# Performance work log

Measured on AMD Instinct MI355X. Metric: run time of the kernel, lower is better.

The kernel has to match this reference:

```python
import jax, jax.numpy as jnp
import numpy as np

DIM = 2048
HEADS = 16
HD = DIM // HEADS
B = 1
S = 2560
L_CAP = 256
NAG_SCALE = 5.0
NAG_ALPHA = 0.25
NAG_TAU = 2.5
EPS_RMS = 1e-5


def setup_inputs() -> dict:
    key = jax.random.key(0)
    ks = jax.random.split(key, 6)
    h = jax.random.normal(ks[0], (B, S, DIM), dtype=jnp.float32)
    wq = jax.random.normal(ks[1], (DIM, DIM), dtype=jnp.float32) * 0.02
    wk = jax.random.normal(ks[2], (DIM, DIM), dtype=jnp.float32) * 0.02
    wv = jax.random.normal(ks[3], (DIM, DIM), dtype=jnp.float32) * 0.02
    wo = jax.random.normal(ks[4], (DIM, DIM), dtype=jnp.float32) * 0.02
    norm_q_w = jnp.ones((HD,), dtype=jnp.float32)
    norm_k_w = jnp.ones((HD,), dtype=jnp.float32)
    # real rotary angles: freqs_cis[b, s, d, 0]=cos, [...,1]=sin
    pos = jnp.arange(S, dtype=jnp.float32)[:, None]          # [S,1]
    inv_freq = 1.0 / (10000.0 ** (jnp.arange(HD // 2, dtype=jnp.float32) / (HD // 2)))
    ang = pos * inv_freq                                      # [S, HD/2]
    freqs_cis = jnp.stack([jnp.cos(ang), jnp.sin(ang)], axis=-1)[None]  # [1,S,HD/2,2]
    return {"h": h, "wq": wq, "wk": wk, "wv": wv, "wo": wo,
            "norm_q_w": norm_q_w, "norm_k_w": norm_k_w,
            "freqs_cis": freqs_cis, "cap_embed_len": L_CAP}


def _rmsnorm(x, w):
    # over last (head) dim
    return x * jax.lax.rsqrt(jnp.mean(x * x, axis=-1, keepdims=True) + EPS_RMS) * w


def _rope(x, freqs_cis):
    # x: [B,S,H,D]; freqs_cis: [1,S,D/2,2]
    xr = x.reshape(*x.shape[:-1], -1, 2)      # [B,S,H,D/2,2]
    cos = freqs_cis[..., 0][:, :, None, :]    # [1,S,1,D/2]
    sin = freqs_cis[..., 1][:, :, None, :]
    x0, x1 = xr[..., 0], xr[..., 1]
    o0 = x0 * cos - x1 * sin
    o1 = x1 * cos + x0 * sin
    return jnp.stack([o0, o1], axis=-1).reshape(x.shape)


def _sdpa(q, k, v):
    # q,k,v: [B,N,H,D] -> [B,N,H*D]
    scale = 1.0 / jnp.sqrt(jnp.asarray(q.shape[-1], q.dtype))
    s = jnp.einsum('bnhd,bmhd->bhnm', q, k) * scale
    a = jax.nn.softmax(s, axis=-1)
    o = jnp.einsum('bhnm,bmhd->bnhd', a, v)
    return o.reshape(o.shape[0], o.shape[1], -1)


def reference(h, wq, wk, wv, wo, norm_q_w, norm_k_w, freqs_cis, cap_embed_len):
    b, s, dim = h.shape
    q = (h @ wq.T).reshape(b, s, HEADS, HD)
    k = (h @ wk.T).reshape(b, s, HEADS, HD)
    v = (h @ wv.T).reshape(b, s, HEADS, HD)
    q = _rmsnorm(q, norm_q_w)
    k = _rmsnorm(k, norm_k_w)
    q = _rope(q, freqs_cis)
    k = _rope(k, freqs_cis)

    L = cap_embed_len
    # positive pass: drop trailing negative-caption tokens
    x_pos = _sdpa(q[:, :-L], k[:, :-L], v[:, :-L])            # [B,S-L,DIM]
    # swap positive caption slot for the negative caption
    q2 = q.at[:, -2 * L:-L].set(q[:, -L:])
    k2 = k.at[:, -2 * L:-L].set(k[:, -L:])
    v2 = v.at[:, -2 * L:-L].set(v[:, -L:])
    x_neg = _sdpa(q2[:, :-L], k2[:, :-L], v2[:, :-L])         # [B,S-L,DIM]
    x_neg_tail = x_neg[:, -L:]

    x_g = x_neg * (1.0 - NAG_SCALE) + x_pos * NAG_SCALE
    norm_pos = jnp.sum(jnp.abs(x_pos), axis=-1, keepdims=True)
    norm_g = jnp.sum(jnp.abs(x_g), axis=-1, keepdims=True)
    ratio = jnp.nan_to_num(norm_g / norm_pos, nan=10.0)
    factor = (1.0 / (norm_g + 1e-7)) * norm_pos * NAG_TAU
    x_g = jnp.where(ratio > NAG_TAU, x_g * factor, x_g)
    x_g = x_g * NAG_ALPHA + x_pos * (1.0 - NAG_ALPHA)

    out = jnp.concatenate([x_g, x_neg_tail], axis=1)          # [B,S,DIM]
    return out @ wo.T
```

## Files before the change

kernel.cpp:

```cpp
#include <hip/hip_runtime.h>
#include <stdint.h>


typedef short s8x __attribute__((ext_vector_type(8)));
typedef float f4x __attribute__((ext_vector_type(4)));
typedef unsigned short u16;

#define NDIM   2048
#define NHEAD  16
#define NHD    128
#define NSEQ   2560
#define NSDPA  2304

__device__ __forceinline__ u16 f2bf(float f) {
  union { float f; unsigned u; } v; v.f = f;
  unsigned r = v.u + 0x7FFFu + ((v.u >> 16) & 1u);
  return (u16)(r >> 16);
}

__device__ __forceinline__ float bf2f(unsigned hi16_in_place) {
  union { unsigned u; float f; } v; v.u = hi16_in_place;
  return v.f;
}

__device__ __forceinline__ void gload16(const void* g, void* l) {
  __builtin_amdgcn_global_load_lds(
      (const __attribute__((address_space(1))) unsigned*)g,
      (__attribute__((address_space(3))) unsigned*)l, 16, 0, 0);
}

__global__ void k_cast(const float* __restrict__ h, const float* __restrict__ w0,
                       const float* __restrict__ w1, const float* __restrict__ w2,
                       const float* __restrict__ w3, u16* __restrict__ hB,
                       u16* __restrict__ wB) {
  int bid = blockIdx.x;
  const float* src; u16* dst; int i;
  if (bid < 2560) {
    src = h; dst = hB; i = bid * 256 + threadIdx.x;
  } else {
    int b = bid - 2560;
    int m = b >> 11;
    i = (b & 2047) * 256 + threadIdx.x;
    src = (m == 0) ? w0 : (m == 1) ? w1 : (m == 2) ? w2 : w3;
    dst = wB + (size_t)m * 4194304;
  }
  const float4* s4 = (const float4*)src + (size_t)i * 2;
  float4 a = s4[0], b4 = s4[1];
  uint4 p;
  p.x = (unsigned)f2bf(a.x) | ((unsigned)f2bf(a.y) << 16);
  p.y = (unsigned)f2bf(a.z) | ((unsigned)f2bf(a.w) << 16);
  p.z = (unsigned)f2bf(b4.x) | ((unsigned)f2bf(b4.y) << 16);
  p.w = (unsigned)f2bf(b4.z) | ((unsigned)f2bf(b4.w) << 16);
  *(uint4*)(dst + (size_t)i * 8) = p;
}

__global__ __launch_bounds__(256, 2)
void k_gemm_bt(const u16* __restrict__ A, const u16* __restrict__ B,
               float* __restrict__ C, int K, int ldc, int nbn) {
  __shared__ __align__(16) unsigned char sm[16384];
  const int cpx = gridDim.x >> 3;
  const int f = blockIdx.x;
  const int swz = (f & 7) * cpx + (f >> 3);
  const int bm = (swz / nbn) * 128, bn = (swz % nbn) * 128;
  const int lane = threadIdx.x & 63, wl = threadIdx.x >> 6;
  const int wm = wl >> 1, wn = wl & 1;
  const int g = lane >> 4, li = lane & 15;
  f4x acc[4][4] = {};
  const int nk = K >> 5;
  for (int kk = 0; kk < nk; ++kk) {
#pragma unroll
    for (int c = 0; c < 2; ++c) {
      int base = (wl * 2 + c) * 1024;
      int row = (base >> 6) + (lane >> 2);
      int colb = (lane & 3) * 16;
      gload16((const char*)A + ((size_t)(bm + row) * K + kk * 32) * 2 + colb, sm + base);
      gload16((const char*)B + ((size_t)(bn + row) * K + kk * 32) * 2 + colb, sm + 8192 + base);
    }
    __syncthreads();
    s8x a[4];
#pragma unroll
    for (int mt = 0; mt < 4; ++mt)
      a[mt] = *(const s8x*)(sm + (wm * 64 + mt * 16 + li) * 64 + g * 16);
#pragma unroll
    for (int nt = 0; nt < 4; ++nt) {
      s8x b = *(const s8x*)(sm + 8192 + (wn * 64 + nt * 16 + li) * 64 + g * 16);
#pragma unroll
      for (int mt = 0; mt < 4; ++mt)
        acc[mt][nt] = __builtin_amdgcn_mfma_f32_16x16x32_bf16(a[mt], b, acc[mt][nt], 0, 0, 0);
    }
    __syncthreads();
  }
#pragma unroll
  for (int mt = 0; mt < 4; ++mt)
#pragma unroll
    for (int nt = 0; nt < 4; ++nt)
#pragma unroll
      for (int r = 0; r < 4; ++r) {
        int row = bm + wm * 64 + mt * 16 + g * 4 + r;
        int col = bn + wn * 64 + nt * 16 + li;
        C[(size_t)row * ldc + col] = acc[mt][nt][r];
      }
}

__device__ __forceinline__ void stageAB256(const u16* __restrict__ M, int K,
                                           int row0, int kk, unsigned char* dst,
                                           int tid) {
#pragma unroll
  for (int c = 0; c < 4; ++c) {
    int idx = c * 512 + tid;
    int r = idx >> 3, cc = idx & 7;
    gload16(M + (size_t)(row0 + r) * K + kk + ((cc ^ (r & 7)) * 8), dst + idx * 16);
  }
}

#define G256_SYNC() do { __builtin_amdgcn_s_barrier();                        \
    asm volatile("s_waitcnt lgkmcnt(0)" ::: "memory");                        \
    __builtin_amdgcn_sched_barrier(0); } while (0)

__global__ __launch_bounds__(512, 2)
void k_gemm256(const u16* __restrict__ A, const u16* __restrict__ B,
               u16* __restrict__ C, u16* __restrict__ vT,
               int K, int ldc, int nbn) {
  extern __shared__ __align__(16) unsigned char sm[];
  const int tid = threadIdx.x;
  const int lane = tid & 63, wid = tid >> 6;
  const int g = lane >> 4, li = lane & 15;
  const int wr = wid >> 2, wc = wid & 3;

  const int cpx = gridDim.x >> 3;
  const int f = blockIdx.x;
  const int swz = (f & 7) * cpx + (f >> 3);
  const int bm = (swz / nbn) * 256, bn = (swz % nbn) * 256;

  f4x acc[8][4] = {};
  const int nk = K >> 6;

  stageAB256(A, K, bm, 0, sm, tid);
  stageAB256(B, K, bn, 0, sm + 32768, tid);
  stageAB256(A, K, bm, 64, sm + 65536, tid);
  stageAB256(B, K, bn, 64, sm + 98304, tid);
  asm volatile("s_waitcnt vmcnt(8)" ::: "memory");
  __builtin_amdgcn_s_barrier();

  for (int t = 0; t < nk; ++t) {
    unsigned char* sA = sm + (t & 1) * 65536;
    unsigned char* sB = sA + 32768;
    s8x a[8][2], b[4][2];

#pragma unroll
    for (int mt = 0; mt < 4; ++mt) {
      int r = wr * 128 + mt * 16 + li;
#pragma unroll
      for (int ks = 0; ks < 2; ++ks)
        a[mt][ks] = *(const s8x*)(sA + r * 128 + (((ks * 4 + g) ^ (r & 7)) * 16));
    }
#pragma unroll
    for (int nt = 0; nt < 4; ++nt) {
      int r = wc * 64 + nt * 16 + li;
      b[nt][0] = *(const s8x*)(sB + r * 128 + ((g ^ (r & 7)) * 16));
    }
    G256_SYNC();
    __builtin_amdgcn_s_setprio(1);
#pragma unroll
    for (int nt = 0; nt < 4; ++nt)
#pragma unroll
      for (int mt = 0; mt < 4; ++mt)
        acc[mt][nt] = __builtin_amdgcn_mfma_f32_16x16x32_bf16(a[mt][0], b[nt][0], acc[mt][nt], 0, 0, 0);
    __builtin_amdgcn_s_setprio(0);
    __builtin_amdgcn_s_barrier();

#pragma unroll
    for (int mt = 4; mt < 8; ++mt) {
      int r = wr * 128 + mt * 16 + li;
#pragma unroll
      for (int ks = 0; ks < 2; ++ks)
        a[mt][ks] = *(const s8x*)(sA + r * 128 + (((ks * 4 + g) ^ (r & 7)) * 16));
    }
#pragma unroll
    for (int nt = 0; nt < 4; ++nt) {
      int r = wc * 64 + nt * 16 + li;
      b[nt][1] = *(const s8x*)(sB + r * 128 + (((4 + g) ^ (r & 7)) * 16));
    }
    G256_SYNC();
    __builtin_amdgcn_s_setprio(1);
#pragma unroll
    for (int nt = 0; nt < 4; ++nt)
#pragma unroll
      for (int mt = 4; mt < 8; ++mt)
        acc[mt][nt] = __builtin_amdgcn_mfma_f32_16x16x32_bf16(a[mt][0], b[nt][0], acc[mt][nt], 0, 0, 0);
    __builtin_amdgcn_s_setprio(0);
    __builtin_amdgcn_s_barrier();

    if (t + 2 < nk) stageAB256(A, K, bm, (t + 2) * 64, sA, tid);
    G256_SYNC();
    __builtin_amdgcn_s_setprio(1);
#pragma unroll
    for (int nt = 0; nt < 4; ++nt)
#pragma unroll
      for (int mt = 0; mt < 4; ++mt)
        acc[mt][nt] = __builtin_amdgcn_mfma_f32_16x16x32_bf16(a[mt][1], b[nt][1], acc[mt][nt], 0, 0, 0);
    __builtin_amdgcn_s_setprio(0);
    __builtin_amdgcn_s_barrier();

    if (t + 2 < nk) stageAB256(B, K, bn, (t + 2) * 64, sB, tid);
    G256_SYNC();
    __builtin_amdgcn_s_setprio(1);
#pragma unroll
    for (int nt = 0; nt < 4; ++nt)
#pragma unroll
      for (int mt = 4; mt < 8; ++mt)
        acc[mt][nt] = __builtin_amdgcn_mfma_f32_16x16x32_bf16(a[mt][1], b[nt][1], acc[mt][nt], 0, 0, 0);
    __builtin_amdgcn_s_setprio(0);
    if (t + 1 < nk) {
      if (t + 2 < nk) asm volatile("s_waitcnt vmcnt(8)" ::: "memory");
      else            asm volatile("s_waitcnt vmcnt(0)" ::: "memory");
      __builtin_amdgcn_s_barrier();
    }
  }

  if (bn < 4096) {
#pragma unroll
    for (int mt = 0; mt < 8; ++mt)
#pragma unroll
      for (int nt = 0; nt < 4; ++nt)
#pragma unroll
        for (int rr = 0; rr < 4; ++rr) {
          int row = bm + wr * 128 + mt * 16 + g * 4 + rr;
          int col = bn + wc * 64 + nt * 16 + li;
          C[(size_t)row * ldc + col] = f2bf(acc[mt][nt][rr]);
        }
  } else {
    __syncthreads();
#pragma unroll
    for (int mt = 0; mt < 8; ++mt)
#pragma unroll
      for (int nt = 0; nt < 4; ++nt) {
        int col = wc * 64 + nt * 16 + li;
        int rowb = (wr * 128 + mt * 16 + g * 4) * 2;
        u16 pk[4];
#pragma unroll
        for (int rr = 0; rr < 4; ++rr) pk[rr] = f2bf(acc[mt][nt][rr]);
        uint2 w;
        w.x = (unsigned)pk[0] | ((unsigned)pk[1] << 16);
        w.y = (unsigned)pk[2] | ((unsigned)pk[3] << 16);
        *(uint2*)(sm + col * 512 + (rowb ^ ((col & 7) << 4))) = w;
      }
    __syncthreads();
    const int hbase = (bn - 4096) >> 7;
#pragma unroll
    for (int c = 0; c < 16; ++c) {
      int idx = c * 512 + tid;
      int col = idx >> 5, ch = idx & 31;
      uint4 v = *(const uint4*)(sm + col * 512 + ((ch * 16) ^ ((col & 7) << 4)));
      int hh = hbase + (col >> 7);
      int d = col & 127;
      *(uint4*)(vT + ((size_t)hh * 128 + d) * NSEQ + bm + ch * 8) = v;
    }
  }
}

__global__ void k_prep(const u16* __restrict__ qkv, const float* __restrict__ nqw,
                       const float* __restrict__ nkw, const float* __restrict__ fc,
                       u16* __restrict__ qh, u16* __restrict__ kh) {
  int wid = threadIdx.x >> 6, lane = threadIdx.x & 63;
  int pair = blockIdx.x * 4 + wid;
  int s = pair >> 4, hh = pair & 15;
  const u16* qrow = qkv + (size_t)s * 6144 + hh * 128;
  unsigned uq = *(const unsigned*)(qrow + lane * 2);
  unsigned uk = *(const unsigned*)(qrow + 2048 + lane * 2);
  float qx = bf2f(uq << 16), qy = bf2f(uq & 0xFFFF0000u);
  float kx = bf2f(uk << 16), ky = bf2f(uk & 0xFFFF0000u);
  float sq = qx * qx + qy * qy;
  float sk = kx * kx + ky * ky;
#pragma unroll
  for (int m = 32; m >= 1; m >>= 1) { sq += __shfl_xor(sq, m); sk += __shfl_xor(sk, m); }
  float rq = rsqrtf(sq * (1.f / 128.f) + 1e-5f);
  float rk = rsqrtf(sk * (1.f / 128.f) + 1e-5f);
  float2 wq2 = *(const float2*)(nqw + lane * 2);
  float2 wk2 = *(const float2*)(nkw + lane * 2);
  float2 cs = *(const float2*)(fc + (size_t)s * 128 + lane * 2);
  float q0 = qx * rq * wq2.x, q1 = qy * rq * wq2.y;
  float k0 = kx * rk * wk2.x, k1 = ky * rk * wk2.y;
  unsigned qo = (unsigned)f2bf(q0 * cs.x - q1 * cs.y) | ((unsigned)f2bf(q1 * cs.x + q0 * cs.y) << 16);
  unsigned ko = (unsigned)f2bf(k0 * cs.x - k1 * cs.y) | ((unsigned)f2bf(k1 * cs.x + k0 * cs.y) << 16);
  *(unsigned*)(qh + ((size_t)hh * NSEQ + s) * 128 + lane * 2) = qo;
  *(unsigned*)(kh + ((size_t)hh * NSEQ + s) * 128 + lane * 2) = ko;
}

__device__ __forceinline__ void stage_kv(const u16* __restrict__ khh,
                                         const u16* __restrict__ vTh,
                                         int kphys, unsigned char* sm,
                                         int lane, int wl) {
#pragma unroll
  for (int c = 0; c < 4; ++c) {
    int base = (wl * 4 + c) * 1024;
    { int row = (base >> 8) + (lane >> 4);
      int src = ((lane & 15) * 16) ^ ((row & 7) << 4);
      gload16((const char*)(khh + (size_t)(kphys + row) * 128) + src, sm + base); }
    { int row = (base >> 7) + (lane >> 3);
      int src = ((lane & 7) * 16) ^ ((row & 7) << 4);
      gload16((const char*)(vTh + (size_t)row * NSEQ + kphys) + src, sm + 16384 + base); }
  }
}

__device__ __forceinline__ void tile_compute(unsigned char* sm, unsigned char* pb,
                                             const s8x (&aq)[4], int g, int li,
                                             f4x (&o)[9], float& mold) {
  const float S2 = 0.08838834764831845f * 1.4426950408889634f;
  const float THR_RAW = 90.0f;
  const s8x PONE = {16256, 16256, 16256, 16256, 16256, 16256, 16256, 16256};
  const f4x zf = {0.f, 0.f, 0.f, 0.f};
  f4x sc[4];
#pragma unroll
  for (int nt = 0; nt < 4; ++nt) sc[nt] = zf;
  __builtin_amdgcn_s_setprio(1);
#pragma unroll
  for (int nt = 0; nt < 4; ++nt) {
    int row = nt * 16 + li;
    int rx = (row & 7) << 4;
#pragma unroll
    for (int ds = 0; ds < 4; ++ds) {
      s8x bk = *(const s8x*)(sm + row * 256 + ((ds * 64 + g * 16) ^ rx));
      sc[nt] = __builtin_amdgcn_mfma_f32_16x16x32_bf16(bk, aq[ds], sc[nt], 0, 0, 0);
    }
  }
  __builtin_amdgcn_s_setprio(0);

  float tl = fmaxf(fmaxf(fmaxf(sc[0][0], sc[0][1]), fmaxf(sc[0][2], sc[0][3])),
                   fmaxf(fmaxf(sc[1][0], sc[1][1]), fmaxf(sc[1][2], sc[1][3])));
  tl = fmaxf(tl, fmaxf(fmaxf(fmaxf(sc[2][0], sc[2][1]), fmaxf(sc[2][2], sc[2][3])),
                       fmaxf(fmaxf(sc[3][0], sc[3][1]), fmaxf(sc[3][2], sc[3][3]))));
  tl = fmaxf(tl, __shfl_xor(tl, 16));
  tl = fmaxf(tl, __shfl_xor(tl, 32));
  if (__any((int)(tl > mold + THR_RAW))) {
    float mn = fmaxf(mold, tl);
    float corr = exp2f((mold - mn) * S2);
    mold = mn;
    float cf[4];
#pragma unroll
    for (int r = 0; r < 4; ++r)
      cf[r] = __shfl(corr, (g << 4) | (g * 4 + r));
#pragma unroll
    for (int dt = 0; dt < 9; ++dt)
#pragma unroll
      for (int r = 0; r < 4; ++r) o[dt][r] *= cf[r];
  }
  float nb = -mold * S2;
#pragma unroll
  for (int nt = 0; nt < 4; ++nt) {
    u16 pp[4];
#pragma unroll
    for (int r = 0; r < 4; ++r) {
      float p = exp2f(fmaf(sc[nt][r], S2, nb));
      union { float f; unsigned u; } pv_; pv_.f = p;
      pp[r] = (u16)(pv_.u >> 16);
    }
    uint2 w;
    w.x = (unsigned)pp[0] | ((unsigned)pp[1] << 16);
    w.y = (unsigned)pp[2] | ((unsigned)pp[3] << 16);
    *(uint2*)(pb + li * 128 + ((nt * 32 + g * 8) ^ ((li & 7) << 4))) = w;
  }
  __builtin_amdgcn_s_setprio(1);
#pragma unroll
  for (int ks = 0; ks < 2; ++ks) {
    s8x pa = *(const s8x*)(pb + li * 128 + ((ks * 64 + g * 16) ^ ((li & 7) << 4)));
#pragma unroll
    for (int dt = 0; dt < 8; ++dt) {
      int row = dt * 16 + li;
      s8x bv = *(const s8x*)(sm + 16384 + row * 128 + ((ks * 64 + g * 16) ^ ((row & 7) << 4)));
      o[dt] = __builtin_amdgcn_mfma_f32_16x16x32_bf16(pa, bv, o[dt], 0, 0, 0);
    }
    o[8] = __builtin_amdgcn_mfma_f32_16x16x32_bf16(pa, PONE, o[8], 0, 0, 0);
  }
  __builtin_amdgcn_s_setprio(0);
}

__device__ __forceinline__ void epilogue(u16* __restrict__ out, int q0, int hh,
                                         int g, int li, const f4x (&o)[9]) {
  float inv[4];
#pragma unroll
  for (int r = 0; r < 4; ++r) inv[r] = 1.f / o[8][r];
#pragma unroll
  for (int dt = 0; dt < 8; ++dt)
#pragma unroll
    for (int r = 0; r < 4; ++r) {
      int n = q0 + g * 4 + r;
      int col = hh * 128 + dt * 16 + li;
      out[(size_t)n * NDIM + col] = f2bf(o[dt][r] * inv[r]);
    }
}

__global__ __launch_bounds__(256, 3)
void k_attn(const u16* __restrict__ qh, const u16* __restrict__ kh,
            const u16* __restrict__ vT, u16* __restrict__ xpos,
            u16* __restrict__ xneg) {
  __shared__ __align__(16) unsigned char sm[40960];
  const int lane = threadIdx.x & 63, wl = threadIdx.x >> 6;
  const int g = lane >> 4, li = lane & 15;

  const int s = blockIdx.x;
  const int xcd = s & 7, j = s >> 3;
  const int hh = 2 * xcd + (j & 1);
  const int u = j >> 1;
  const bool shared_blk = (u < 32);
  const int qb = shared_blk ? u : (32 + ((u - 32) >> 1));
  const int mode = shared_blk ? 0 : ((u - 32) & 1);
  const int q0 = qb * 64 + wl * 16;

  const u16* khh = kh + (size_t)hh * NSEQ * 128;
  const u16* vTh = vT + (size_t)hh * 128 * NSEQ;
  unsigned char* pb = sm + 32768 + wl * 2048;

  s8x aq[4];
  {
    int ql = q0 + li;
    int qp = (mode && ql >= 2048) ? ql + 256 : ql;
    const u16* base = qh + ((size_t)hh * NSEQ + qp) * 128 + g * 8;
#pragma unroll
    for (int ds = 0; ds < 4; ++ds) aq[ds] = *(const s8x*)(base + ds * 32);
  }

  const f4x zf = {0.f, 0.f, 0.f, 0.f};
  f4x o1[9];
  float m1 = -1e30f;
#pragma unroll
  for (int dt = 0; dt < 9; ++dt) o1[dt] = zf;

  const int n1 = shared_blk ? 32 : 36;
  for (int t = 0; t < n1; ++t) {
    int kphys = (mode && t >= 32) ? 2304 + (t - 32) * 64 : t * 64;
    stage_kv(khh, vTh, kphys, sm, lane, wl);
    __syncthreads();
    tile_compute(sm, pb, aq, g, li, o1, m1);
    __syncthreads();
  }

  if (shared_blk) {
    f4x o2[9];
    float m2 = m1;
#pragma unroll
    for (int dt = 0; dt < 9; ++dt) o2[dt] = o1[dt];
    for (int t = 0; t < 4; ++t) {
      stage_kv(khh, vTh, 2048 + t * 64, sm, lane, wl);
      __syncthreads();
      tile_compute(sm, pb, aq, g, li, o1, m1);
      __syncthreads();
    }
    epilogue(xpos, q0, hh, g, li, o1);
    for (int t = 0; t < 4; ++t) {
      stage_kv(khh, vTh, 2304 + t * 64, sm, lane, wl);
      __syncthreads();
      tile_compute(sm, pb, aq, g, li, o2, m2);
      __syncthreads();
    }
    epilogue(xneg, q0, hh, g, li, o2);
  } else {
    epilogue(mode ? xneg : xpos, q0, hh, g, li, o1);
  }
}

__global__ void k_nag(const u16* __restrict__ xp, const u16* __restrict__ xn,
                      u16* __restrict__ X) {
  int n = blockIdx.x, t = threadIdx.x;
  if (n >= NSDPA) {
    *(uint4*)(X + (size_t)n * NDIM + t * 8) =
        *(const uint4*)(xn + (size_t)(n - 256) * NDIM + t * 8);
    return;
  }
  uint4 up = *(const uint4*)(xp + (size_t)n * NDIM + t * 8);
  uint4 un = *(const uint4*)(xn + (size_t)n * NDIM + t * 8);
  unsigned wp[4] = {up.x, up.y, up.z, up.w};
  unsigned wn[4] = {un.x, un.y, un.z, un.w};
  float pv[8], nv[8], gv[8];
#pragma unroll
  for (int i = 0; i < 4; ++i) {
    pv[2 * i] = bf2f(wp[i] << 16);  pv[2 * i + 1] = bf2f(wp[i] & 0xFFFF0000u);
    nv[2 * i] = bf2f(wn[i] << 16);  nv[2 * i + 1] = bf2f(wn[i] & 0xFFFF0000u);
  }
  float sp = 0.f, sg = 0.f;
#pragma unroll
  for (int i = 0; i < 8; ++i) {
    float gq = 5.f * pv[i] - 4.f * nv[i];
    gv[i] = gq; sp += fabsf(pv[i]); sg += fabsf(gq);
  }
#pragma unroll
  for (int m = 32; m >= 1; m >>= 1) { sp += __shfl_xor(sp, m); sg += __shfl_xor(sg, m); }
  __shared__ float red[2][4];
  int wid = t >> 6, lane = t & 63;
  if (lane == 0) { red[0][wid] = sp; red[1][wid] = sg; }
  __syncthreads();
  float np_ = red[0][0] + red[0][1] + red[0][2] + red[0][3];
  float ng_ = red[1][0] + red[1][1] + red[1][2] + red[1][3];
  float ratio = ng_ / np_;
  if (isnan(ratio)) ratio = 10.f;
  float factor = np_ * 2.5f / (ng_ + 1e-7f);
  float mul = (ratio > 2.5f) ? factor : 1.f;
  uint4 p;
  u16 ob[8];
#pragma unroll
  for (int i = 0; i < 8; ++i) ob[i] = f2bf(gv[i] * mul * 0.25f + pv[i] * 0.75f);
  p.x = (unsigned)ob[0] | ((unsigned)ob[1] << 16);
  p.y = (unsigned)ob[2] | ((unsigned)ob[3] << 16);
  p.z = (unsigned)ob[4] | ((unsigned)ob[5] << 16);
  p.w = (unsigned)ob[6] | ((unsigned)ob[7] << 16);
  *(uint4*)(X + (size_t)n * NDIM + t * 8) = p;
}

extern "C" void kernel_launch(void* const* d_in, const int* in_sizes, int n_in,
                              void* d_out, int out_size, void* d_ws, size_t ws_size,
                              hipStream_t stream) {
  const float* h   = (const float*)d_in[0];
  const float* wq  = (const float*)d_in[1];
  const float* wk  = (const float*)d_in[2];
  const float* wv  = (const float*)d_in[3];
  const float* wo  = (const float*)d_in[4];
  const float* nqw = (const float*)d_in[5];
  const float* nkw = (const float*)d_in[6];
  const float* fc  = (const float*)d_in[7];
  (void)in_sizes; (void)n_in; (void)out_size; (void)ws_size;

  char* ws = (char*)d_ws;
  u16*   wB   = (u16*)ws;
  u16*   hB   = (u16*)(ws + 33554432);
  u16*   qkvb = (u16*)(ws + 44040192);
  u16*   qh   = (u16*)(ws + 106954752);
  u16*   kh   = qh + (size_t)16 * 2560 * 128;
  u16*   vT   = kh + (size_t)16 * 2560 * 128;
  u16*   xpos = (u16*)(ws + 44040192);
  u16*   xneg = xpos + (size_t)NSDPA * NDIM;
  u16*   X    = hB;

  static bool attr_done = false;
  if (!attr_done) {
    hipFuncSetAttribute((const void*)k_gemm256,
                        hipFuncAttributeMaxDynamicSharedMemorySize, 131072);
    attr_done = true;
  }

  k_cast<<<10752, 256, 0, stream>>>(h, wq, wk, wv, wo, hB, wB);
  k_gemm256<<<240, 512, 131072, stream>>>(hB, wB, qkvb, vT, 2048, 6144, 24);
  k_prep<<<10240, 256, 0, stream>>>(qkvb, nqw, nkw, fc, qh, kh);
  k_attn<<<640, 256, 0, stream>>>(qh, kh, vT, xpos, xneg);
  k_nag<<<2560, 256, 0, stream>>>(xpos, xneg, X);
  k_gemm_bt<<<320, 256, 0, stream>>>(X, wB + 12582912, (float*)d_out, 2048, 2048, 16);
}
```

Measured before the change: 238.4 us.

## Simplify 256-tile GEMM main loop to single LDS read phase then bulk prefetch

Replaces the four-phase interleaved schedule in the 256x256 GEMM (fragment reads, barriers and partial global prefetches spread between MFMA groups) with one phase. It reads all A/B fragments for the k-step, runs all 64 MFMAs, then issues both A and B prefetches after a single barrier. This removes three barriers and their lgkmcnt waits per iteration. The cost is more live fragment registers and less overlap between global loads and MFMA work within an iteration.

```diff
diff --git a/kernel.cpp b/kernel.cpp
--- a/kernel.cpp
+++ b/kernel.cpp
@@ -113,10 +113,6 @@
   }
 }
 
-#define G256_SYNC() do { __builtin_amdgcn_s_barrier();                        \
-    asm volatile("s_waitcnt lgkmcnt(0)" ::: "memory");                        \
-    __builtin_amdgcn_sched_barrier(0); } while (0)
-
 __global__ __launch_bounds__(512, 2)
 void k_gemm256(const u16* __restrict__ A, const u16* __restrict__ B,
                u16* __restrict__ C, u16* __restrict__ vT,
@@ -141,6 +137,7 @@
   stageAB256(B, K, bn, 64, sm + 98304, tid);
   asm volatile("s_waitcnt vmcnt(8)" ::: "memory");
   __builtin_amdgcn_s_barrier();
+  __builtin_amdgcn_sched_barrier(0);
 
   for (int t = 0; t < nk; ++t) {
     unsigned char* sA = sm + (t & 1) * 65536;
@@ -148,7 +145,7 @@
     s8x a[8][2], b[4][2];
 
 #pragma unroll
-    for (int mt = 0; mt < 4; ++mt) {
+    for (int mt = 0; mt < 8; ++mt) {
       int r = wr * 128 + mt * 16 + li;
 #pragma unroll
       for (int ks = 0; ks < 2; ++ks)
@@ -157,64 +154,34 @@
 #pragma unroll
     for (int nt = 0; nt < 4; ++nt) {
       int r = wc * 64 + nt * 16 + li;
-      b[nt][0] = *(const s8x*)(sB + r * 128 + ((g ^ (r & 7)) * 16));
-    }
-    G256_SYNC();
+#pragma unroll
+      for (int ks = 0; ks < 2; ++ks)
+        b[nt][ks] = *(const s8x*)(sB + r * 128 + (((ks * 4 + g) ^ (r & 7)) * 16));
+    }
     __builtin_amdgcn_s_setprio(1);
 #pragma unroll
-    for (int nt = 0; nt < 4; ++nt)
-#pragma unroll
-      for (int mt = 0; mt < 4; ++mt)
-        acc[mt][nt] = __builtin_amdgcn_mfma_f32_16x16x32_bf16(a[mt][0], b[nt][0], acc[mt][nt], 0, 0, 0);
+    for (int ks = 0; ks < 2; ++ks)
+#pragma unroll
+      for (int half = 0; half < 2; ++half)
+#pragma unroll
+        for (int nt = 0; nt < 4; ++nt)
+#pragma unroll
+          for (int mt = half * 4; mt < half * 4 + 4; ++mt)
+            acc[mt][nt] = __builtin_amdgcn_mfma_f32_16x16x32_bf16(
+                a[mt][ks], b[nt][ks], acc[mt][nt], 0, 0, 0);
     __builtin_amdgcn_s_setprio(0);
+
     __builtin_amdgcn_s_barrier();
-
-#pragma unroll
-    for (int mt = 4; mt < 8; ++mt) {
-      int r = wr * 128 + mt * 16 + li;
-#pragma unroll
-      for (int ks = 0; ks < 2; ++ks)
-        a[mt][ks] = *(const s8x*)(sA + r * 128 + (((ks * 4 + g) ^ (r & 7)) * 16));
-    }
-#pragma unroll
-    for (int nt = 0; nt < 4; ++nt) {
-      int r = wc * 64 + nt * 16 + li;
-      b[nt][1] = *(const s8x*)(sB + r * 128 + (((4 + g) ^ (r & 7)) * 16));
-    }
-    G256_SYNC();
-    __builtin_amdgcn_s_setprio(1);
-#pragma unroll
-    for (int nt = 0; nt < 4; ++nt)
-#pragma unroll
-      for (int mt = 4; mt < 8; ++mt)
-        acc[mt][nt] = __builtin_amdgcn_mfma_f32_16x16x32_bf16(a[mt][0], b[nt][0], acc[mt][nt], 0, 0, 0);
-    __builtin_amdgcn_s_setprio(0);
-    __builtin_amdgcn_s_barrier();
-
-    if (t + 2 < nk) stageAB256(A, K, bm, (t + 2) * 64, sA, tid);
-    G256_SYNC();
-    __builtin_amdgcn_s_setprio(1);
-#pragma unroll
-    for (int nt = 0; nt < 4; ++nt)
-#pragma unroll
-      for (int mt = 0; mt < 4; ++mt)
-        acc[mt][nt] = __builtin_amdgcn_mfma_f32_16x16x32_bf16(a[mt][1], b[nt][1], acc[mt][nt], 0, 0, 0);
-    __builtin_amdgcn_s_setprio(0);
-    __builtin_amdgcn_s_barrier();
-
-    if (t + 2 < nk) stageAB256(B, K, bn, (t + 2) * 64, sB, tid);
-    G256_SYNC();
-    __builtin_amdgcn_s_setprio(1);
-#pragma unroll
-    for (int nt = 0; nt < 4; ++nt)
-#pragma unroll
-      for (int mt = 4; mt < 8; ++mt)
-        acc[mt][nt] = __builtin_amdgcn_mfma_f32_16x16x32_bf16(a[mt][1], b[nt][1], acc[mt][nt], 0, 0, 0);
-    __builtin_amdgcn_s_setprio(0);
+    __builtin_amdgcn_sched_barrier(0);
+    if (t + 2 < nk) {
+      stageAB256(A, K, bm, (t + 2) * 64, sA, tid);
+      stageAB256(B, K, bn, (t + 2) * 64, sB, tid);
+    }
     if (t + 1 < nk) {
       if (t + 2 < nk) asm volatile("s_waitcnt vmcnt(8)" ::: "memory");
       else            asm volatile("s_waitcnt vmcnt(0)" ::: "memory");
       __builtin_amdgcn_s_barrier();
+      __builtin_amdgcn_sched_barrier(0);
     }
   }
 
```

Measured after the change: 239.8 us. About the same (+0.6%).
